# Performance work log

Measured on AMD Instinct MI355X. Metric: run time of the kernel, lower is better.

## Reference

```python
import jax, jax.numpy as jnp
import numpy as np

# Hyperparameters (from init_kwargs)
D_MODEL = 1024
D_STATE = 64
HEADDIM = 64
MIMO_RANK = 2
CHUNK = 128
EXPAND = 2
D_INNER = EXPAND * D_MODEL            # 2048
NHEADS = D_INNER // HEADDIM           # 32
G = MIMO_RANK * D_STATE               # effective state channels per head = 128
D_CONV = 4
D_XBC = D_INNER + 2 * NHEADS * G      # conv channels
D_IN_PROJ = 2 * D_INNER + 2 * NHEADS * G + NHEADS  # [z, x, B, C, dt]


def rmsnorm(x, w, eps=1e-5):
    return x * w * jax.lax.rsqrt(jnp.mean(x * x, axis=-1, keepdims=True) + eps)


def setup_inputs() -> dict:
    key = jax.random.key(0)
    ks = jax.random.split(key, 8)
    B, L = 2, 2048
    x = jax.random.normal(ks[0], (B, L, D_MODEL), jnp.float32)
    norm_w = jnp.ones((D_MODEL,), jnp.float32)
    in_proj_w = jax.random.normal(ks[1], (D_IN_PROJ, D_MODEL), jnp.float32) * 0.02
    conv_w = jax.random.normal(ks[2], (D_XBC, D_CONV), jnp.float32) * 0.2
    conv_b = jnp.zeros((D_XBC,), jnp.float32)
    dt_bias = jax.random.uniform(ks[3], (NHEADS,), jnp.float32, minval=-4.0, maxval=-1.0)
    A_log = jnp.log(jax.random.uniform(ks[4], (NHEADS,), jnp.float32, minval=1.0, maxval=8.0))
    D_skip = jnp.ones((NHEADS,), jnp.float32)
    gnorm_w = jnp.ones((D_INNER,), jnp.float32)
    out_proj_w = jax.random.normal(ks[5], (D_MODEL, D_INNER), jnp.float32) * 0.02
    return dict(x=x, norm_w=norm_w, in_proj_w=in_proj_w, conv_w=conv_w, conv_b=conv_b,
                dt_bias=dt_bias, A_log=A_log, D_skip=D_skip, gnorm_w=gnorm_w,
                out_proj_w=out_proj_w)


def _mamba3(u, in_proj_w, conv_w, conv_b, dt_bias, A_log, D_skip, gnorm_w, out_proj_w):
    B, L, _ = u.shape
    H, P = NHEADS, HEADDIM
    nc = L // CHUNK

    zxbcdt = u @ in_proj_w.T                                   # (B,L,D_IN_PROJ)
    z, xbc, dt_raw = jnp.split(zxbcdt, [D_INNER, D_INNER + D_XBC], axis=-1)

    # causal depthwise conv (width D_CONV) + SiLU on [x, B, C]
    xp = jnp.pad(xbc, ((0, 0), (D_CONV - 1, 0), (0, 0)))
    conv = conv_b + sum(xp[:, k:k + L, :] * conv_w[:, k] for k in range(D_CONV))
    xbc = jax.nn.silu(conv)
    xh, Bm, Cm = jnp.split(xbc, [D_INNER, D_INNER + H * G], axis=-1)

    Xc = xh.reshape(B, nc, CHUNK, H, P)
    Bc = Bm.reshape(B, nc, CHUNK, H, G)
    Cc = Cm.reshape(B, nc, CHUNK, H, G)

    dt = jax.nn.softplus(dt_raw + dt_bias)                     # (B,L,H), positive
    A = -jnp.exp(A_log)                                        # (H,), negative
    dtc = dt.reshape(B, nc, CHUNK, H)
    a = dtc * A                                                # log decay, (B,nc,cs,H)
    cum = jnp.cumsum(a, axis=2)                                # inclusive cumsum within chunk

    # intra-chunk (quadratic, causal) part
    cumT = cum.transpose(0, 1, 3, 2)                           # (B,nc,H,cs)
    diff = cumT[..., :, None] - cumT[..., None, :]             # cum_l - cum_s
    mask = jnp.tril(jnp.ones((CHUNK, CHUNK), bool))
    decay = jnp.where(mask, jnp.exp(jnp.where(mask, diff, 0.0)), 0.0)
    dtT = dtc.transpose(0, 1, 3, 2)                            # (B,nc,H,cs)
    scores = jnp.einsum('bclhg,bcshg->bchls', Cc, Bc) * decay * dtT[:, :, :, None, :]
    Y_intra = jnp.einsum('bchls,bcshp->bclhp', scores, Xc)

    # inter-chunk state recurrence
    w = jnp.exp(cum[:, :, -1:, :] - cum) * dtc                 # (B,nc,cs,H)
    S = jnp.einsum('bcshg,bcshp->bchgp', Bc * w[..., None], Xc)  # chunk states
    dlast = jnp.exp(cum[:, :, -1, :])                          # (B,nc,H) total chunk decay

    def step(carry, inp):
        dl, s = inp
        return dl[:, :, None, None] * carry + s, carry

    init = jnp.zeros((B, H, G, P), u.dtype)
    _, Hprev = jax.lax.scan(step, init, (dlast.transpose(1, 0, 2), S.transpose(1, 0, 2, 3, 4)))
    Hprev = Hprev.transpose(1, 0, 2, 3, 4)                     # (B,nc,H,G,P) state before chunk
    Y_inter = jnp.einsum('bclhg,bchgp->bclhp', Cc * jnp.exp(cum)[..., None], Hprev)

    y = (Y_intra + Y_inter + D_skip[:, None] * Xc).reshape(B, L, D_INNER)
    y = rmsnorm(y * jax.nn.silu(z), gnorm_w)                   # gated RMSNorm
    return y @ out_proj_w.T


def reference(x, norm_w, in_proj_w, conv_w, conv_b, dt_bias, A_log, D_skip, gnorm_w, out_proj_w):
    # pre-norm residual wrapper
    return x + _mamba3(rmsnorm(x, norm_w), in_proj_w, conv_w, conv_b,
                       dt_bias, A_log, D_skip, gnorm_w, out_proj_w)
```

## Files before the change

kernel.cpp:

```cpp
#include <hip/hip_runtime.h>

typedef unsigned short u16;
typedef __attribute__((ext_vector_type(8))) short bf16x8;
typedef __attribute__((ext_vector_type(4))) float f32x4;

#define MFMA16(a,b,c) __builtin_amdgcn_mfma_f32_16x16x32_bf16(a,b,c,0,0,0)

#define DMODEL   1024
#define DINNER   2048
#define NHEADS   32
#define HEADDIM  64
#define GDIM     128
#define DXBC     10240
#define DPROJ    12320
#define CHUNK_L  128
#define NCHUNK   16
#define NROWS    4096

__device__ __forceinline__ float b2f(u16 u){ return __uint_as_float(((unsigned)u)<<16); }
__device__ __forceinline__ u16 f2b(float f){
  unsigned u = __float_as_uint(f);
  u += 0x7fffu + ((u>>16)&1u);
  return (u16)(u>>16);
}

__device__ __forceinline__ void gload_lds16(const void* g, void* l){
  __builtin_amdgcn_global_load_lds(
      (const __attribute__((address_space(1))) unsigned int*)g,
      (__attribute__((address_space(3))) unsigned int*)l, 16, 0, 0);
}

__global__ __launch_bounds__(256) void k_prep(const float* __restrict__ s1, u16* __restrict__ d1, int n1,
                                              const float* __restrict__ s2, u16* __restrict__ d2, int n2,
                                              const float* __restrict__ x, const float* __restrict__ w,
                                              u16* __restrict__ u){
  __shared__ float red[4];
  if (blockIdx.x < 2048){
    int i = blockIdx.x*256 + threadIdx.x;
    int stride = 2048*256;
    int t1 = n1 >> 2, t2 = n2 >> 2;
    for (int j=i; j<t1+t2; j+=stride){
      const float4* sp; uint2* dp; int idx;
      if (j < t1){ sp = (const float4*)s1; dp = (uint2*)d1; idx = j; }
      else       { sp = (const float4*)s2; dp = (uint2*)d2; idx = j - t1; }
      float4 v = sp[idx];
      uint2 o;
      o.x = (unsigned)f2b(v.x) | ((unsigned)f2b(v.y)<<16);
      o.y = (unsigned)f2b(v.z) | ((unsigned)f2b(v.w)<<16);
      dp[idx] = o;
    }
  } else {
    int row = blockIdx.x - 2048, tid = threadIdx.x;
    float4 v = reinterpret_cast<const float4*>(x + (size_t)row*DMODEL)[tid];
    float ss = v.x*v.x + v.y*v.y + v.z*v.z + v.w*v.w;
    #pragma unroll
    for (int off=32; off>0; off>>=1) ss += __shfl_down(ss, off, 64);
    if ((tid&63)==0) red[tid>>6] = ss;
    __syncthreads();
    float tot = red[0]+red[1]+red[2]+red[3];
    float sc = rsqrtf(tot/(float)DMODEL + 1e-5f);
    float4 wv = reinterpret_cast<const float4*>(w)[tid];
    uint2 o;
    o.x = (unsigned)f2b(v.x*wv.x*sc) | ((unsigned)f2b(v.y*wv.y*sc)<<16);
    o.y = (unsigned)f2b(v.z*wv.z*sc) | ((unsigned)f2b(v.w*wv.w*sc)<<16);
    reinterpret_cast<uint2*>(u + (size_t)row*DMODEL)[tid] = o;
  }
}

__global__ __launch_bounds__(512) void k_gemm1_8p(const u16* __restrict__ A,
                                                  const u16* __restrict__ W,
                                                  u16* __restrict__ zb,
                                                  u16* __restrict__ xbc){
  __shared__ __align__(16) u16 lds[65536];
  const int tid  = threadIdx.x;
  const int lane = tid & 63, w = tid >> 6;
  const int wr = w >> 2, wc = w & 3;
  int bid = blockIdx.x;
  int xcd = bid & 7, g = bid >> 3;
  int st  = xcd*6 + (g >> 4);
  int wi  = g & 15;
  int tm  = (st/12)*4 + (wi>>2);
  int tn  = (st%12)*4 + (wi&3);
  const int m0 = tm*256, n0 = tn*256;

  const int srow = w*8 + (lane>>3);
  const int scol = ((lane&7) ^ ((lane>>3)&7))*8;
  const u16* aS = A + (size_t)(m0 + srow)*DMODEL + scol;
  const u16* bS = W + (size_t)(n0 + srow)*DMODEL + scol;
  const int ldsw = w*512;

  const int rr = lane & 15, gq = lane >> 4;

  f32x4 acc[8][4];
  #pragma unroll
  for (int i=0;i<8;i++)
    #pragma unroll
    for (int j=0;j<4;j++) acc[i][j] = (f32x4){0,0,0,0};

  auto SU_A = [&](int kt, int j){
    gload_lds16(aS + (size_t)(j*64)*DMODEL + kt*64,
                lds + (kt&1)*32768 + j*4096 + ldsw);
  };
  auto SU_B = [&](int kt, int j){
    gload_lds16(bS + (size_t)(j*64)*DMODEL + kt*64,
                lds + (kt&1)*32768 + 16384 + j*4096 + ldsw);
  };

  SU_A(0,0); SU_A(0,2); SU_B(0,0); SU_B(0,2); SU_B(0,1); SU_B(0,3); SU_A(0,1); SU_A(0,3);
  asm volatile("s_waitcnt vmcnt(2)" ::: "memory");
  __builtin_amdgcn_s_barrier();
  __builtin_amdgcn_sched_barrier(0);

  for (int kt = 0; kt < 16; ++kt){
    const u16* bufA = lds + (kt&1)*32768;
    const u16* bufB = bufA + 16384;
    const bool stg = (kt < 15);
    bf16x8 af[4][2], bw0[2][2], bw1[2][2];

    auto RDA = [&](int ti, int ks)->bf16x8{
      int r = wr*128 + ti*16 + rr;
      int s = (ks*4 + gq) ^ (rr & 7);
      return *(const bf16x8*)&bufA[r*64 + s*8];
    };
    auto RDB = [&](int tj, int ks)->bf16x8{
      int r = wc*64 + tj*16 + rr;
      int s = (ks*4 + gq) ^ (rr & 7);
      return *(const bf16x8*)&bufB[r*64 + s*8];
    };

    #pragma unroll
    for (int ti=0;ti<4;ti++){ af[ti][0]=RDA(ti,0); af[ti][1]=RDA(ti,1); }
    #pragma unroll
    for (int tj=0;tj<2;tj++){ bw0[tj][0]=RDB(tj,0); bw0[tj][1]=RDB(tj,1); }
    if (stg){ SU_A(kt+1,0); SU_A(kt+1,2); }
    __builtin_amdgcn_s_barrier();
    asm volatile("s_waitcnt lgkmcnt(0)" ::: "memory");
    __builtin_amdgcn_sched_barrier(0);
    __builtin_amdgcn_s_setprio(1);
    #pragma unroll
    for (int ti=0;ti<4;ti++)
      #pragma unroll
      for (int tj=0;tj<2;tj++){
        acc[ti][tj] = MFMA16(af[ti][0], bw0[tj][0], acc[ti][tj]);
        acc[ti][tj] = MFMA16(af[ti][1], bw0[tj][1], acc[ti][tj]);
      }
    __builtin_amdgcn_s_setprio(0);
    __builtin_amdgcn_s_barrier();

    #pragma unroll
    for (int tj=0;tj<2;tj++){ bw1[tj][0]=RDB(tj+2,0); bw1[tj][1]=RDB(tj+2,1); }
    if (stg){ SU_B(kt+1,0); SU_B(kt+1,2); }
    __builtin_amdgcn_s_barrier();
    asm volatile("s_waitcnt lgkmcnt(0)" ::: "memory");
    __builtin_amdgcn_sched_barrier(0);
    __builtin_amdgcn_s_setprio(1);
    #pragma unroll
    for (int ti=0;ti<4;ti++)
      #pragma unroll
      for (int tj=0;tj<2;tj++){
        acc[ti][tj+2] = MFMA16(af[ti][0], bw1[tj][0], acc[ti][tj+2]);
        acc[ti][tj+2] = MFMA16(af[ti][1], bw1[tj][1], acc[ti][tj+2]);
      }
    __builtin_amdgcn_s_setprio(0);
    if (stg) asm volatile("s_waitcnt vmcnt(4)" ::: "memory");
    else     asm volatile("s_waitcnt vmcnt(0)" ::: "memory");
    __builtin_amdgcn_s_barrier();

    #pragma unroll
    for (int ti=0;ti<4;ti++){ af[ti][0]=RDA(ti+4,0); af[ti][1]=RDA(ti+4,1); }
    if (stg){ SU_B(kt+1,1); SU_B(kt+1,3); }
    __builtin_amdgcn_s_barrier();
    asm volatile("s_waitcnt lgkmcnt(0)" ::: "memory");
    __builtin_amdgcn_sched_barrier(0);
    __builtin_amdgcn_s_setprio(1);
    #pragma unroll
    for (int ti=0;ti<4;ti++)
      #pragma unroll
      for (int tj=0;tj<2;tj++){
        acc[4+ti][tj] = MFMA16(af[ti][0], bw0[tj][0], acc[4+ti][tj]);
        acc[4+ti][tj] = MFMA16(af[ti][1], bw0[tj][1], acc[4+ti][tj]);
      }
    __builtin_amdgcn_s_setprio(0);
    __builtin_amdgcn_s_barrier();

    if (stg){ SU_A(kt+1,1); SU_A(kt+1,3); }
    __builtin_amdgcn_s_barrier();
    __builtin_amdgcn_sched_barrier(0);
    __builtin_amdgcn_s_setprio(1);
    #pragma unroll
    for (int ti=0;ti<4;ti++)
      #pragma unroll
      for (int tj=0;tj<2;tj++){
        acc[4+ti][tj+2] = MFMA16(af[ti][0], bw1[tj][0], acc[4+ti][tj+2]);
        acc[4+ti][tj+2] = MFMA16(af[ti][1], bw1[tj][1], acc[4+ti][tj+2]);
      }
    __builtin_amdgcn_s_setprio(0);
    if (stg){
      asm volatile("s_waitcnt vmcnt(2)" ::: "memory");
      __builtin_amdgcn_s_barrier();
      __builtin_amdgcn_sched_barrier(0);
    }
  }

  const int row0 = m0 + wr*128 + (lane>>4)*4;
  const int colb = wc*64 + (lane&15);
  if (tn >= 8){
    const int cb = n0 - DINNER;
    #pragma unroll
    for (int ti=0;ti<8;ti++)
      #pragma unroll
      for (int tj=0;tj<4;tj++)
        #pragma unroll
        for (int q=0;q<4;q++)
          xbc[(size_t)(row0 + ti*16 + q)*DXBC + cb + colb + tj*16] = f2b(acc[ti][tj][q]);
  } else {
    #pragma unroll
    for (int ti=0;ti<8;ti++)
      #pragma unroll
      for (int tj=0;tj<4;tj++)
        #pragma unroll
        for (int q=0;q<4;q++)
          zb[(size_t)(row0 + ti*16 + q)*DINNER + n0 + colb + tj*16] = f2b(acc[ti][tj][q]);
  }
}

__global__ __launch_bounds__(256) void k_gemm_dt(const u16* __restrict__ A,
                                                 const u16* __restrict__ W,
                                                 float* __restrict__ dtraw){
  const int lane = threadIdx.x & 63, wv = threadIdx.x >> 6;
  const int m0 = blockIdx.x*32;
  const int n0 = DINNER + DXBC;
  const int r  = lane & 15;
  const int kb = (lane>>4)*8;
  const int k0 = wv*256;
  const u16* a0p = A + (size_t)(m0 + r)*DMODEL + k0 + kb;
  const u16* a1p = a0p + 16*DMODEL;
  const u16* b0p = W + (size_t)(n0 + r)*DMODEL + k0 + kb;
  const u16* b1p = b0p + 16*DMODEL;
  f32x4 acc00={0,0,0,0}, acc01={0,0,0,0}, acc10={0,0,0,0}, acc11={0,0,0,0};
  #pragma unroll
  for (int k=0;k<256;k+=32){
    bf16x8 a0 = *(const bf16x8*)(a0p + k);
    bf16x8 a1 = *(const bf16x8*)(a1p + k);
    bf16x8 b0 = *(const bf16x8*)(b0p + k);
    bf16x8 b1 = *(const bf16x8*)(b1p + k);
    acc00 = MFMA16(a0,b0,acc00);
    acc01 = MFMA16(a0,b1,acc01);
    acc10 = MFMA16(a1,b0,acc10);
    acc11 = MFMA16(a1,b1,acc11);
  }
  __shared__ float part[4][1024];
  int rowb = (lane>>4)*4, col = lane&15;
  #pragma unroll
  for (int rr=0; rr<4; rr++){
    part[wv][(rowb+rr)*32 + col]         = acc00[rr];
    part[wv][(rowb+rr)*32 + col+16]      = acc01[rr];
    part[wv][(rowb+16+rr)*32 + col]      = acc10[rr];
    part[wv][(rowb+16+rr)*32 + col+16]   = acc11[rr];
  }
  __syncthreads();
  int idx = threadIdx.x*4;
  #pragma unroll
  for (int q=0;q<4;q++){
    int i = idx+q;
    dtraw[(size_t)m0*NHEADS + i] = part[0][i]+part[1][i]+part[2][i]+part[3][i];
  }
}

__global__ __launch_bounds__(128) void k_dtscan(const float* __restrict__ dtraw,
                                                const float* __restrict__ dt_bias,
                                                const float* __restrict__ A_log,
                                                float* __restrict__ dtT,
                                                float* __restrict__ cumT){
  int blk = blockIdx.x;
  int h   = blk & 31;
  int bc  = blk >> 5;
  int s   = threadIdx.x;
  int row = bc*128 + s;
  float xv = dtraw[(size_t)row*NHEADS + h] + dt_bias[h];
  float dt = (xv > 20.f) ? xv : log1pf(expf(xv));
  float a  = dt * (-expf(A_log[h]));
  __shared__ float lds[128];
  lds[s] = a; __syncthreads();
  #pragma unroll
  for (int off=1; off<128; off<<=1){
    float t = (s>=off) ? lds[s-off] : 0.f;
    __syncthreads();
    lds[s] += t;
    __syncthreads();
  }
  dtT[(size_t)blk*128 + s]  = dt;
  cumT[(size_t)blk*128 + s] = lds[s];
}

__global__ __launch_bounds__(256) void k_conv(const u16* __restrict__ xbc,
                                              const float* __restrict__ cw,
                                              const float* __restrict__ cb,
                                              u16* __restrict__ xh,
                                              u16* __restrict__ Bm,
                                              u16* __restrict__ Cm){
  int c  = (blockIdx.x*256 + threadIdx.x)*2;
  int row0 = blockIdx.y*16;
  int l0 = row0 & 2047;
  float4 wa = reinterpret_cast<const float4*>(cw)[c];
  float4 wb = reinterpret_cast<const float4*>(cw)[c+1];
  float cba = cb[c], cbb = cb[c+1];
  float a3=0,a2=0,a1=0, b3=0,b2=0,b1=0;
  auto loadpair = [&](int rw, float& fa, float& fb){
    unsigned v = *(const unsigned*)&xbc[(size_t)rw*DXBC + c];
    fa = b2f((u16)v); fb = b2f((u16)(v>>16));
  };
  if (l0 >= 3){
    loadpair(row0-3, a3,b3); loadpair(row0-2, a2,b2); loadpair(row0-1, a1,b1);
  }
  #pragma unroll
  for (int i=0;i<16;i++){
    float a0,b0; loadpair(row0+i, a0,b0);
    float sa = cba + a3*wa.x + a2*wa.y + a1*wa.z + a0*wa.w;
    float sb = cbb + b3*wb.x + b2*wb.y + b1*wb.z + b0*wb.w;
    sa = sa/(1.f+expf(-sa)); sb = sb/(1.f+expf(-sb));
    unsigned o = (unsigned)f2b(sa) | ((unsigned)f2b(sb)<<16);
    int rw = row0 + i;
    if (c < DINNER)            *(unsigned*)&xh[(size_t)rw*DINNER + c] = o;
    else if (c < DINNER+4096)  *(unsigned*)&Bm[(size_t)rw*4096 + (c-DINNER)] = o;
    else                       *(unsigned*)&Cm[(size_t)rw*4096 + (c-DINNER-4096)] = o;
    a3=a2; a2=a1; a1=a0; b3=b2; b2=b1; b1=b0;
  }
}

__global__ __launch_bounds__(512) void k_states(const u16* __restrict__ Bm,
                                                const u16* __restrict__ xh,
                                                const float* __restrict__ dtT,
                                                const float* __restrict__ cumT,
                                                u16* __restrict__ S){
  int blk = blockIdx.x;
  int h = blk & 31, bc = blk >> 5;
  __shared__ __align__(16) u16 Bw[128][136];
  __shared__ __align__(16) u16 XT[64][136];
  __shared__ float cum[128], dtv[128];
  int tid = threadIdx.x;
  if (tid < 128){ cum[tid] = cumT[(size_t)blk*128+tid]; dtv[tid] = dtT[(size_t)blk*128+tid]; }
  __syncthreads();
  float clast = cum[127];
  #pragma unroll
  for (int it=0; it<4; ++it){
    int s  = it*32 + (tid>>4);
    int g8 = (tid&15)*8;
    uint4 v = *(const uint4*)&Bm[(size_t)(bc*128+s)*4096 + h*128 + g8];
    float w = expf(clast - cum[s]) * dtv[s];
    const u16* pv = (const u16*)&v;
    #pragma unroll
    for (int j=0;j<8;j++) Bw[g8+j][s] = f2b(b2f(pv[j]) * w);
  }
  #pragma unroll
  for (int it=0; it<4; ++it){
    int s  = it*32 + (tid>>4);
    int p4 = (tid&15)*4;
    uint2 v = *(const uint2*)&xh[(size_t)(bc*128+s)*DINNER + h*64 + p4];
    const u16* pv = (const u16*)&v;
    #pragma unroll
    for (int j=0;j<4;j++) XT[p4+j][s] = pv[j];
  }
  __syncthreads();
  int lane = tid & 63, wv = tid >> 6;
  int r = lane & 15, kb = (lane>>4)*8;
  f32x4 acc[4];
  #pragma unroll
  for (int j=0;j<4;j++) acc[j] = (f32x4){0,0,0,0};
  #pragma unroll
  for (int k=0;k<128;k+=32){
    bf16x8 a0 = *(const bf16x8*)&Bw[wv*16 + r][k+kb];
    #pragma unroll
    for (int tj=0;tj<4;tj++){
      bf16x8 bb = *(const bf16x8*)&XT[tj*16 + r][k+kb];
      acc[tj] = MFMA16(a0,bb,acc[tj]);
    }
  }
  u16* Sp = S + (size_t)blk*8192;
  int g0 = wv*16 + (lane>>4)*4, p0 = lane&15;
  #pragma unroll
  for (int tj=0;tj<4;tj++)
    #pragma unroll
    for (int rr=0;rr<4;rr++)
      Sp[(g0 + rr)*64 + tj*16 + p0] = f2b(acc[tj][rr]);
}

__global__ __launch_bounds__(256) void k_scan(const u16* __restrict__ S,
                                              const float* __restrict__ cumT,
                                              u16* __restrict__ Hp){
  int slice = blockIdx.x & 3;
  int bh = blockIdx.x >> 2;
  int b = bh >> 5, h = bh & 31;
  int e0 = slice*2048 + threadIdx.x*8;
  float c8[8];
  #pragma unroll
  for (int j=0;j<8;j++) c8[j] = 0.f;
  for (int c=0;c<NCHUNK;c++){
    int blk = (b*16+c)*32 + h;
    float dl = expf(cumT[(size_t)blk*128 + 127]);
    uint4 sv = *(const uint4*)&S[(size_t)blk*8192 + e0];
    const u16* sp = (const u16*)&sv;
    uint4 o; u16* op = (u16*)&o;
    #pragma unroll
    for (int j=0;j<8;j++) op[j] = f2b(c8[j]);
    *reinterpret_cast<uint4*>(&Hp[(size_t)blk*8192 + e0]) = o;
    #pragma unroll
    for (int j=0;j<8;j++) c8[j] = dl*c8[j] + b2f(sp[j]);
  }
}

__global__ __launch_bounds__(512) void k_intra(const u16* __restrict__ Cm,
                                               const u16* __restrict__ Bm,
                                               const u16* __restrict__ xh,
                                               const u16* __restrict__ Hp,
                                               const float* __restrict__ dtT,
                                               const float* __restrict__ cumT,
                                               const float* __restrict__ Dskip,
                                               u16* __restrict__ yh){
  int blk = blockIdx.x;
  int h = blk & 31, bc = blk >> 5;
  __shared__ __align__(16) u16 Bl[128][136];
  __shared__ __align__(16) u16 XT[64][136];
  __shared__ __align__(16) u16 HT[64][136];
  __shared__ float cum[128], dtv[128];
  int tid = threadIdx.x;
  int lane = tid & 63, wv = tid >> 6;
  int r = lane & 15, kb = (lane>>4)*8;

  bf16x8 cfr[4];
  {
    const u16* cp = Cm + (size_t)(bc*128 + wv*16 + r)*4096 + h*128 + kb;
    #pragma unroll
    for (int ks=0;ks<4;ks++) cfr[ks] = *(const bf16x8*)(cp + ks*32);
  }

  if (tid < 128){ cum[tid] = cumT[(size_t)blk*128+tid]; dtv[tid] = dtT[(size_t)blk*128+tid]; }
  #pragma unroll
  for (int it=0; it<4; ++it){
    int rw = it*32 + (tid>>4);
    int g8 = (tid&15)*8;
    *(uint4*)&Bl[rw][g8] = *(const uint4*)&Bm[(size_t)(bc*128+rw)*4096 + h*128 + g8];
  }
  #pragma unroll
  for (int it=0; it<4; ++it){
    int s  = it*32 + (tid>>4);
    int p4 = (tid&15)*4;
    uint2 v = *(const uint2*)&xh[(size_t)(bc*128+s)*DINNER + h*64 + p4];
    const u16* pv = (const u16*)&v;
    #pragma unroll
    for (int j=0;j<4;j++) XT[p4+j][s] = pv[j];
  }
  #pragma unroll
  for (int it=0; it<4; ++it){
    int g  = it*32 + (tid>>4);
    int p4 = (tid&15)*4;
    uint2 v = *(const uint2*)&Hp[(size_t)blk*8192 + g*64 + p4];
    const u16* pv = (const u16*)&v;
    #pragma unroll
    for (int j=0;j<4;j++) HT[p4+j][g] = pv[j];
  }
  __syncthreads();
  const int tjmax = wv;

  f32x4 p1[8];
  #pragma unroll
  for (int j=0;j<8;j++) p1[j] = (f32x4){0,0,0,0};
  #pragma unroll
  for (int ks=0;ks<4;ks++){
    bf16x8 a0 = cfr[ks];
    #pragma unroll
    for (int tj=0;tj<8;tj++){
      if (tj > tjmax) continue;
      bf16x8 bb = *(const bf16x8*)&Bl[tj*16 + r][ks*32+kb];
      p1[tj] = MFMA16(a0,bb,p1[tj]);
    }
  }
  __syncthreads();
  int row0 = wv*16 + (lane>>4)*4;
  #pragma unroll
  for (int tj=0;tj<8;tj++)
    #pragma unroll
    for (int rr=0;rr<4;rr++){
      int l = row0 + rr;
      int s = tj*16 + (lane&15);
      float v = p1[tj][rr];
      v = (s <= l) ? v * expf(cum[l]-cum[s]) * dtv[s] : 0.f;
      Bl[l][s] = f2b(v);
    }
  __syncthreads();

  f32x4 y[4];
  #pragma unroll
  for (int j=0;j<4;j++) y[j] = (f32x4){0,0,0,0};
  #pragma unroll
  for (int ks=0;ks<4;ks++){
    bf16x8 a0 = cfr[ks];
    #pragma unroll
    for (int tj=0;tj<4;tj++){
      bf16x8 bb = *(const bf16x8*)&HT[tj*16 + r][ks*32+kb];
      y[tj] = MFMA16(a0,bb,y[tj]);
    }
  }
  #pragma unroll
  for (int rr=0;rr<4;rr++){
    float e = expf(cum[row0 + rr]);
    #pragma unroll
    for (int tj=0;tj<4;tj++) y[tj][rr] *= e;
  }
  #pragma unroll
  for (int k=0;k<128;k+=32){
    bf16x8 a0 = *(const bf16x8*)&Bl[wv*16 + r][k+kb];
    #pragma unroll
    for (int tj=0;tj<4;tj++){
      bf16x8 bb = *(const bf16x8*)&XT[tj*16 + r][k+kb];
      y[tj] = MFMA16(a0,bb,y[tj]);
    }
  }
  float Dh = Dskip[h];
  #pragma unroll
  for (int tj=0;tj<4;tj++)
    #pragma unroll
    for (int rr=0;rr<4;rr++){
      int l = row0 + rr;
      int p = tj*16 + (lane&15);
      float xv = b2f(XT[p][l]);
      yh[(size_t)(bc*128 + l)*DINNER + h*64 + p] = f2b(y[tj][rr] + Dh*xv);
    }
}

__global__ __launch_bounds__(256) void k_gate(const u16* __restrict__ yh,
                                              const u16* __restrict__ zb,
                                              const float* __restrict__ gw,
                                              u16* __restrict__ out){
  int row = blockIdx.x, tid = threadIdx.x;
  const uint4 yv = reinterpret_cast<const uint4*>(yh + (size_t)row*DINNER)[tid];
  const uint4 zv = reinterpret_cast<const uint4*>(zb + (size_t)row*DINNER)[tid];
  const unsigned* yp = (const unsigned*)&yv;
  const unsigned* zp = (const unsigned*)&zv;
  float t[8]; float ss = 0.f;
  #pragma unroll
  for (int i=0;i<4;i++){
    float y0 = b2f((u16)yp[i]), y1 = b2f((u16)(yp[i]>>16));
    float z0 = b2f((u16)zp[i]), z1 = b2f((u16)(zp[i]>>16));
    float v0 = y0 * (z0 / (1.f + expf(-z0)));
    float v1 = y1 * (z1 / (1.f + expf(-z1)));
    t[2*i] = v0; t[2*i+1] = v1; ss += v0*v0 + v1*v1;
  }
  #pragma unroll
  for (int off=32; off>0; off>>=1) ss += __shfl_down(ss, off, 64);
  __shared__ float red[4];
  if ((tid&63)==0) red[tid>>6] = ss;
  __syncthreads();
  float tot = red[0]+red[1]+red[2]+red[3];
  float g = rsqrtf(tot/(float)DINNER + 1e-5f);
  const float4 g0 = reinterpret_cast<const float4*>(gw)[tid*2];
  const float4 g1 = reinterpret_cast<const float4*>(gw)[tid*2+1];
  uint4 o;
  unsigned* op = (unsigned*)&o;
  float gg[8] = {g0.x,g0.y,g0.z,g0.w,g1.x,g1.y,g1.z,g1.w};
  #pragma unroll
  for (int i=0;i<4;i++)
    op[i] = (unsigned)f2b(t[2*i]*gg[2*i]*g) | ((unsigned)f2b(t[2*i+1]*gg[2*i+1]*g)<<16);
  reinterpret_cast<uint4*>(out + (size_t)row*DINNER)[tid] = o;
}

__global__ __launch_bounds__(256) void k_gemm2_64(const u16* __restrict__ A,
                                                  const u16* __restrict__ W,
                                                  const float* __restrict__ xres,
                                                  float* __restrict__ out){
  __shared__ __align__(16) u16 lds[2*16384];
  const int tid  = threadIdx.x;
  const int lane = tid & 63, wv = tid >> 6;
  const int wr = wv >> 1, wc = wv & 1;
  const int NWG = 8*32, Q = NWG/8;
  int swz = (blockIdx.x & 7)*Q + (blockIdx.x >> 3);
  int tm = swz / 8, tn = swz % 8;
  int m0 = tm*128, n0 = tn*128;
  const int K = DINNER;

  const int srow = tid >> 3;
  const int sslot = ((tid&7) ^ ((tid>>3)&7))*8;
  const u16* aSrc = A + (size_t)(m0 + srow)*K + sslot;
  const u16* bSrc = W + (size_t)(n0 + srow)*K + sslot;
  const int ldsu = wv*512;

  const int rr = lane & 15, gq = lane >> 4;

  f32x4 acc[4][4];
  #pragma unroll
  for (int i=0;i<4;i++)
    #pragma unroll
    for (int j=0;j<4;j++) acc[i][j] = (f32x4){0,0,0,0};

  auto STAGE = [&](int kt){
    u16* base = lds + (kt&1)*16384;
    #pragma unroll
    for (int j=0;j<4;j++)
      gload_lds16(aSrc + (size_t)(j*32)*K + kt*64, base + j*2048 + ldsu);
    #pragma unroll
    for (int j=0;j<4;j++)
      gload_lds16(bSrc + (size_t)(j*32)*K + kt*64, base + 8192 + j*2048 + ldsu);
  };
  auto KSTEP = [&](int kt, bool stg){
    const u16* bufA = lds + (kt&1)*16384;
    const u16* bufB = bufA + 8192;
    bf16x8 af[4][2], bw[4][2];
    #pragma unroll
    for (int t=0;t<4;t++){
      #pragma unroll
      for (int ks=0;ks<2;ks++){
        int sa = (ks*4 + gq) ^ (rr & 7);
        af[t][ks] = *(const bf16x8*)&bufA[(wr*64 + t*16 + rr)*64 + sa*8];
        bw[t][ks] = *(const bf16x8*)&bufB[(wc*64 + t*16 + rr)*64 + sa*8];
      }
    }
    asm volatile("s_waitcnt lgkmcnt(0)" ::: "memory");
    __builtin_amdgcn_s_barrier();
    if (stg) STAGE(kt+2);
    __builtin_amdgcn_s_setprio(1);
    #pragma unroll
    for (int ti=0;ti<4;ti++)
      #pragma unroll
      for (int tj=0;tj<4;tj++){
        acc[ti][tj] = MFMA16(af[ti][0], bw[tj][0], acc[ti][tj]);
        acc[ti][tj] = MFMA16(af[ti][1], bw[tj][1], acc[ti][tj]);
      }
    __builtin_amdgcn_s_setprio(0);
  };

  STAGE(0); STAGE(1);
  asm volatile("s_waitcnt vmcnt(8)" ::: "memory");
  __builtin_amdgcn_s_barrier();
  __builtin_amdgcn_sched_barrier(0);
  const int NT = K/64;
  for (int kt = 0; kt < NT-2; ++kt){
    KSTEP(kt, true);
    asm volatile("s_waitcnt vmcnt(8)" ::: "memory");
    __builtin_amdgcn_s_barrier();
    __builtin_amdgcn_sched_barrier(0);
  }
  KSTEP(NT-2, false);
  asm volatile("s_waitcnt vmcnt(0)" ::: "memory");
  __builtin_amdgcn_s_barrier();
  __builtin_amdgcn_sched_barrier(0);
  KSTEP(NT-1, false);

  int row0 = m0 + wr*64 + (lane>>4)*4;
  int col0 = n0 + wc*64 + (lane&15);
  #pragma unroll
  for (int ti=0;ti<4;ti++)
    #pragma unroll
    for (int tj=0;tj<4;tj++)
      #pragma unroll
      for (int q=0;q<4;q++){
        size_t idx = (size_t)(row0+ti*16+q)*DMODEL + col0 + tj*16;
        out[idx] = acc[ti][tj][q] + xres[idx];
      }
}

extern "C" void kernel_launch(void* const* d_in, const int* in_sizes, int n_in,
                              void* d_out, int out_size, void* d_ws, size_t ws_size,
                              hipStream_t stream) {
  (void)in_sizes; (void)n_in; (void)out_size; (void)ws_size;
  const float* x         = (const float*)d_in[0];
  const float* norm_w    = (const float*)d_in[1];
  const float* in_proj_w = (const float*)d_in[2];
  const float* conv_w    = (const float*)d_in[3];
  const float* conv_b    = (const float*)d_in[4];
  const float* dt_bias   = (const float*)d_in[5];
  const float* A_log     = (const float*)d_in[6];
  const float* D_skip    = (const float*)d_in[7];
  const float* gnorm_w   = (const float*)d_in[8];
  const float* out_proj_w= (const float*)d_in[9];
  float* out = (float*)d_out;

  char* ws = (char*)d_ws;
  size_t off = 0;
  auto alloc = [&](size_t bytes)->char*{
    char* p = ws + off; off = (off + bytes + 255) & ~(size_t)255; return p;
  };
  u16*   W2    = (u16*)  alloc((size_t)DMODEL*DINNER*2);
  u16*   zb    = (u16*)  alloc((size_t)NROWS*DINNER*2);
  float* dtraw = (float*)alloc((size_t)NROWS*NHEADS*4);
  float* dtT   = (float*)alloc((size_t)1024*128*4);
  float* cumT  = (float*)alloc((size_t)1024*128*4);
  u16*   xhb   = (u16*)  alloc((size_t)NROWS*DINNER*2);
  u16*   Bmb   = (u16*)  alloc((size_t)NROWS*4096*2);
  u16*   Cmb   = (u16*)  alloc((size_t)NROWS*4096*2);
  char*  R1    = alloc((size_t)NROWS*DXBC*2);
  u16*   xbcr  = (u16*)R1;
  u16*   S     = (u16*)R1;
  u16*   Hp    = (u16*)(R1 + (size_t)1024*8192*4);
  u16*   yh    = (u16*)R1;
  char*  R2    = alloc((size_t)DPROJ*DMODEL*2 + (size_t)NROWS*DMODEL*2);
  u16*   W1    = (u16*)R2;
  u16*   u_bf  = (u16*)(R2 + (size_t)DPROJ*DMODEL*2);
  u16*   gated = (u16*)R2;

  k_prep<<<2048+NROWS,256,0,stream>>>(in_proj_w, W1, DPROJ*DMODEL,
                                      out_proj_w, W2, DMODEL*DINNER,
                                      x, norm_w, u_bf);
  k_gemm1_8p<<<768,512,0,stream>>>(u_bf, W1, zb, xbcr);
  k_gemm_dt<<<NROWS/32,256,0,stream>>>(u_bf, W1, dtraw);
  k_conv<<<dim3(DXBC/512, NROWS/16),256,0,stream>>>(xbcr, conv_w, conv_b, xhb, Bmb, Cmb);
  k_dtscan<<<1024,128,0,stream>>>(dtraw, dt_bias, A_log, dtT, cumT);
  k_states<<<1024,512,0,stream>>>(Bmb, xhb, dtT, cumT, S);
  k_scan<<<256,256,0,stream>>>(S, cumT, Hp);
  k_intra<<<1024,512,0,stream>>>(Cmb, Bmb, xhb, Hp, dtT, cumT, D_skip, yh);
  k_gate<<<NROWS,256,0,stream>>>(yh, zb, gnorm_w, gated);
  k_gemm2_64<<<8*32,256,0,stream>>>(gated, W2, x, out);
}
```

Measured before the change: 293.1 us.

## Fuse conv and dt-scan launches, prefetch scan inputs, overlap intra loads

```diff
diff --git a/kernel.cpp b/kernel.cpp
--- a/kernel.cpp
+++ b/kernel.cpp
@@ -267,64 +267,75 @@
   }
 }
 
-__global__ __launch_bounds__(128) void k_dtscan(const float* __restrict__ dtraw,
+__global__ __launch_bounds__(256) void k_convdt(const u16* __restrict__ xbc,
+                                                const float* __restrict__ cw,
+                                                const float* __restrict__ cb,
+                                                u16* __restrict__ xh,
+                                                u16* __restrict__ Bm,
+                                                u16* __restrict__ Cm,
+                                                const float* __restrict__ dtraw,
                                                 const float* __restrict__ dt_bias,
                                                 const float* __restrict__ A_log,
                                                 float* __restrict__ dtT,
                                                 float* __restrict__ cumT){
-  int blk = blockIdx.x;
-  int h   = blk & 31;
-  int bc  = blk >> 5;
-  int s   = threadIdx.x;
-  int row = bc*128 + s;
-  float xv = dtraw[(size_t)row*NHEADS + h] + dt_bias[h];
-  float dt = (xv > 20.f) ? xv : log1pf(expf(xv));
-  float a  = dt * (-expf(A_log[h]));
-  __shared__ float lds[128];
-  lds[s] = a; __syncthreads();
-  #pragma unroll
-  for (int off=1; off<128; off<<=1){
-    float t = (s>=off) ? lds[s-off] : 0.f;
-    __syncthreads();
-    lds[s] += t;
-    __syncthreads();
-  }
-  dtT[(size_t)blk*128 + s]  = dt;
-  cumT[(size_t)blk*128 + s] = lds[s];
-}
-
-__global__ __launch_bounds__(256) void k_conv(const u16* __restrict__ xbc,
-                                              const float* __restrict__ cw,
-                                              const float* __restrict__ cb,
-                                              u16* __restrict__ xh,
-                                              u16* __restrict__ Bm,
-                                              u16* __restrict__ Cm){
-  int c  = (blockIdx.x*256 + threadIdx.x)*2;
-  int row0 = blockIdx.y*16;
-  int l0 = row0 & 2047;
-  float4 wa = reinterpret_cast<const float4*>(cw)[c];
-  float4 wb = reinterpret_cast<const float4*>(cw)[c+1];
-  float cba = cb[c], cbb = cb[c+1];
-  float a3=0,a2=0,a1=0, b3=0,b2=0,b1=0;
-  auto loadpair = [&](int rw, float& fa, float& fb){
-    unsigned v = *(const unsigned*)&xbc[(size_t)rw*DXBC + c];
-    fa = b2f((u16)v); fb = b2f((u16)(v>>16));
-  };
-  if (l0 >= 3){
-    loadpair(row0-3, a3,b3); loadpair(row0-2, a2,b2); loadpair(row0-1, a1,b1);
-  }
-  #pragma unroll
-  for (int i=0;i<16;i++){
-    float a0,b0; loadpair(row0+i, a0,b0);
-    float sa = cba + a3*wa.x + a2*wa.y + a1*wa.z + a0*wa.w;
-    float sb = cbb + b3*wb.x + b2*wb.y + b1*wb.z + b0*wb.w;
-    sa = sa/(1.f+expf(-sa)); sb = sb/(1.f+expf(-sb));
-    unsigned o = (unsigned)f2b(sa) | ((unsigned)f2b(sb)<<16);
-    int rw = row0 + i;
-    if (c < DINNER)            *(unsigned*)&xh[(size_t)rw*DINNER + c] = o;
-    else if (c < DINNER+4096)  *(unsigned*)&Bm[(size_t)rw*4096 + (c-DINNER)] = o;
-    else                       *(unsigned*)&Cm[(size_t)rw*4096 + (c-DINNER-4096)] = o;
-    a3=a2; a2=a1; a1=a0; b3=b2; b2=b1; b1=b0;
+  __shared__ float lds2[2][128];
+  int tid = threadIdx.x;
+  if (blockIdx.x < 2560){
+    int cblk = blockIdx.x;
+    int cx = cblk % 10, ry = cblk / 10;
+    int c0 = (cx*256 + tid)*4;
+    int row0 = ry*16;
+    int l0 = row0 & 2047;
+    float4 w4[4]; float cbv[4];
+    #pragma unroll
+    for (int j=0;j<4;j++){ w4[j] = reinterpret_cast<const float4*>(cw)[c0+j]; cbv[j] = cb[c0+j]; }
+    float p3[4]={0,0,0,0}, p2[4]={0,0,0,0}, p1[4]={0,0,0,0};
+    auto loadquad = [&](int rw, float q[4]){
+      uint2 v = *(const uint2*)&xbc[(size_t)rw*DXBC + c0];
+      const u16* pv = (const u16*)&v;
+      #pragma unroll
+      for (int j=0;j<4;j++) q[j] = b2f(pv[j]);
+    };
+    if (l0 >= 3){ loadquad(row0-3,p3); loadquad(row0-2,p2); loadquad(row0-1,p1); }
+    #pragma unroll
+    for (int i=0;i<16;i++){
+      float cur[4]; loadquad(row0+i, cur);
+      float o[4];
+      #pragma unroll
+      for (int j=0;j<4;j++){
+        float s = cbv[j] + p3[j]*w4[j].x + p2[j]*w4[j].y + p1[j]*w4[j].z + cur[j]*w4[j].w;
+        o[j] = s/(1.f+expf(-s));
+      }
+      uint2 ov;
+      ov.x = (unsigned)f2b(o[0]) | ((unsigned)f2b(o[1])<<16);
+      ov.y = (unsigned)f2b(o[2]) | ((unsigned)f2b(o[3])<<16);
+      int rw = row0 + i;
+      if (c0 < DINNER)            *(uint2*)&xh[(size_t)rw*DINNER + c0] = ov;
+      else if (c0 < DINNER+4096)  *(uint2*)&Bm[(size_t)rw*4096 + (c0-DINNER)] = ov;
+      else                        *(uint2*)&Cm[(size_t)rw*4096 + (c0-DINNER-4096)] = ov;
+      #pragma unroll
+      for (int j=0;j<4;j++){ p3[j]=p2[j]; p2[j]=p1[j]; p1[j]=cur[j]; }
+    }
+  } else {
+    int half = tid >> 7;
+    int blk  = (blockIdx.x - 2560)*2 + half;
+    int h  = blk & 31;
+    int bc = blk >> 5;
+    int s  = tid & 127;
+    int row = bc*128 + s;
+    float xv = dtraw[(size_t)row*NHEADS + h] + dt_bias[h];
+    float dt = (xv > 20.f) ? xv : log1pf(expf(xv));
+    float a  = dt * (-expf(A_log[h]));
+    lds2[half][s] = a; __syncthreads();
+    #pragma unroll
+    for (int off=1; off<128; off<<=1){
+      float t = (s>=off) ? lds2[half][s-off] : 0.f;
+      __syncthreads();
+      lds2[half][s] += t;
+      __syncthreads();
+    }
+    dtT[(size_t)blk*128 + s]  = dt;
+    cumT[(size_t)blk*128 + s] = lds2[half][s];
   }
 }
 
@@ -395,10 +406,17 @@
   float c8[8];
   #pragma unroll
   for (int j=0;j<8;j++) c8[j] = 0.f;
+  int blk0 = (b*16+0)*32 + h;
+  uint4 sv = *(const uint4*)&S[(size_t)blk0*8192 + e0];
+  float dl = expf(cumT[(size_t)blk0*128 + 127]);
   for (int c=0;c<NCHUNK;c++){
+    int blkn = (b*16+c+1)*32 + h;
+    uint4 nx; float dln = 0.f;
+    if (c < NCHUNK-1){
+      nx  = *(const uint4*)&S[(size_t)blkn*8192 + e0];
+      dln = expf(cumT[(size_t)blkn*128 + 127]);
+    }
     int blk = (b*16+c)*32 + h;
-    float dl = expf(cumT[(size_t)blk*128 + 127]);
-    uint4 sv = *(const uint4*)&S[(size_t)blk*8192 + e0];
     const u16* sp = (const u16*)&sv;
     uint4 o; u16* op = (u16*)&o;
     #pragma unroll
@@ -406,6 +424,7 @@
     *reinterpret_cast<uint4*>(&Hp[(size_t)blk*8192 + e0]) = o;
     #pragma unroll
     for (int j=0;j<8;j++) c8[j] = dl*c8[j] + b2f(sp[j]);
+    sv = nx; dl = dln;
   }
 }
 
@@ -441,27 +460,18 @@
     int g8 = (tid&15)*8;
     *(uint4*)&Bl[rw][g8] = *(const uint4*)&Bm[(size_t)(bc*128+rw)*4096 + h*128 + g8];
   }
+  __syncthreads();
+
+  uint2 xt[4], ht[4];
   #pragma unroll
   for (int it=0; it<4; ++it){
     int s  = it*32 + (tid>>4);
     int p4 = (tid&15)*4;
-    uint2 v = *(const uint2*)&xh[(size_t)(bc*128+s)*DINNER + h*64 + p4];
-    const u16* pv = (const u16*)&v;
-    #pragma unroll
-    for (int j=0;j<4;j++) XT[p4+j][s] = pv[j];
-  }
-  #pragma unroll
-  for (int it=0; it<4; ++it){
-    int g  = it*32 + (tid>>4);
-    int p4 = (tid&15)*4;
-    uint2 v = *(const uint2*)&Hp[(size_t)blk*8192 + g*64 + p4];
-    const u16* pv = (const u16*)&v;
-    #pragma unroll
-    for (int j=0;j<4;j++) HT[p4+j][g] = pv[j];
-  }
-  __syncthreads();
+    xt[it] = *(const uint2*)&xh[(size_t)(bc*128+s)*DINNER + h*64 + p4];
+    ht[it] = *(const uint2*)&Hp[(size_t)blk*8192 + (it*32 + (tid>>4))*64 + p4];
+  }
+
   const int tjmax = wv;
-
   f32x4 p1[8];
   #pragma unroll
   for (int j=0;j<8;j++) p1[j] = (f32x4){0,0,0,0};
@@ -475,7 +485,19 @@
       p1[tj] = MFMA16(a0,bb,p1[tj]);
     }
   }
+  #pragma unroll
+  for (int it=0; it<4; ++it){
+    int s  = it*32 + (tid>>4);
+    int p4 = (tid&15)*4;
+    const u16* pv = (const u16*)&xt[it];
+    #pragma unroll
+    for (int j=0;j<4;j++) XT[p4+j][s] = pv[j];
+    const u16* ph = (const u16*)&ht[it];
+    #pragma unroll
+    for (int j=0;j<4;j++) HT[p4+j][it*32 + (tid>>4)] = ph[j];
+  }
   __syncthreads();
+
   int row0 = wv*16 + (lane>>4)*4;
   #pragma unroll
   for (int tj=0;tj<8;tj++)
@@ -700,10 +722,10 @@
   k_prep<<<2048+NROWS,256,0,stream>>>(in_proj_w, W1, DPROJ*DMODEL,
                                       out_proj_w, W2, DMODEL*DINNER,
                                       x, norm_w, u_bf);
+  k_gemm_dt<<<NROWS/32,256,0,stream>>>(u_bf, W1, dtraw);
   k_gemm1_8p<<<768,512,0,stream>>>(u_bf, W1, zb, xbcr);
-  k_gemm_dt<<<NROWS/32,256,0,stream>>>(u_bf, W1, dtraw);
-  k_conv<<<dim3(DXBC/512, NROWS/16),256,0,stream>>>(xbcr, conv_w, conv_b, xhb, Bmb, Cmb);
-  k_dtscan<<<1024,128,0,stream>>>(dtraw, dt_bias, A_log, dtT, cumT);
+  k_convdt<<<2560+512,256,0,stream>>>(xbcr, conv_w, conv_b, xhb, Bmb, Cmb,
+                                      dtraw, dt_bias, A_log, dtT, cumT);
   k_states<<<1024,512,0,stream>>>(Bmb, xhb, dtT, cumT, S);
   k_scan<<<256,256,0,stream>>>(S, cumT, Hp);
   k_intra<<<1024,512,0,stream>>>(Cmb, Bmb, xhb, Hp, dtT, cumT, D_skip, yh);
```

Result: no change. 288.0 us, median of 3 (-1.7%).
